# Optimization experiments

Measured on AMD Instinct MI355X. Metric: run time of the kernel, lower is better.

Reference implementation:

```python
import jax, jax.numpy as jnp
import numpy as np

N_HEADS = 16
N_KV_HEADS = 4
HEAD_DIM = 128


def setup_inputs() -> dict:
    key = jax.random.key(0)
    ks = jax.random.split(key, 5)
    B, T, C = 4, 2048, 2048
    kv_dim = N_KV_HEADS * HEAD_DIM
    s = 0.02
    return {
        "x": jax.random.normal(ks[0], (B, T, C), jnp.float32),
        "Wq": jax.random.normal(ks[1], (C, C), jnp.float32) * s,
        "Wk": jax.random.normal(ks[2], (kv_dim, C), jnp.float32) * s,
        "Wv": jax.random.normal(ks[3], (kv_dim, C), jnp.float32) * s,
        "Wo": jax.random.normal(ks[4], (C, C), jnp.float32) * s,
    }


def reference(x, Wq, Wk, Wv, Wo):
    B, T, C = x.shape
    n_rep = N_HEADS // N_KV_HEADS
    # projections (nn.Linear: y = x @ W^T), reshape to (B, H, T, D)
    q = (x @ Wq.T).reshape(B, T, N_HEADS, HEAD_DIM).transpose(0, 2, 1, 3)
    k = (x @ Wk.T).reshape(B, T, N_KV_HEADS, HEAD_DIM).transpose(0, 2, 1, 3)
    v = (x @ Wv.T).reshape(B, T, N_KV_HEADS, HEAD_DIM).transpose(0, 2, 1, 3)
    # GQA: expand kv heads (repeat_interleave on head dim)
    k = jnp.repeat(k, n_rep, axis=1)
    v = jnp.repeat(v, n_rep, axis=1)
    scale = 1.0 / np.sqrt(HEAD_DIM).astype(np.float32)
    scores = jnp.einsum("bhqd,bhkd->bhqk", q, k) * scale
    causal = jnp.tril(jnp.ones((T, T), bool))
    scores = jnp.where(causal[None, None], scores, -jnp.inf)
    attn = jax.nn.softmax(scores, axis=-1)  # dropout p=0 -> identity
    out = jnp.einsum("bhqk,bhkd->bhqd", attn, v)
    out = out.transpose(0, 2, 1, 3).reshape(B, T, C)
    return out @ Wo.T
```

## Files before the change

### kernel.cpp

```cpp
#include <hip/hip_runtime.h>

#define TB 4
#define TT 2048
#define TC 2048
#define NH 16
#define NKV 4
#define HD 128
#define KVDIM (NKV*HD)
#define NQKV (TC + 2*KVDIM)
#define MTOK (TB*TT)

typedef __bf16 bf16x8 __attribute__((ext_vector_type(8)));
typedef __bf16 bf16x2 __attribute__((ext_vector_type(2)));
typedef float  f32x4  __attribute__((ext_vector_type(4)));
typedef float  f32x16 __attribute__((ext_vector_type(16)));
typedef unsigned short ushort_t;
typedef unsigned short us8 __attribute__((ext_vector_type(8)));
typedef unsigned short us4 __attribute__((ext_vector_type(4)));
typedef unsigned int u32x4 __attribute__((ext_vector_type(4)));
typedef unsigned int u32x2 __attribute__((ext_vector_type(2)));

#define QSC 0.12751743f

__device__ __forceinline__ ushort_t f2bf(float f) {
    unsigned u = __builtin_bit_cast(unsigned, f);
    u += 0x7fffu + ((u >> 16) & 1u);
    return (ushort_t)(u >> 16);
}

__device__ __forceinline__ unsigned pkbf(float lo, float hi) {
    bf16x2 v;
    v[0] = (__bf16)lo; v[1] = (__bf16)hi;
    return __builtin_bit_cast(unsigned, v);
}

__device__ __forceinline__ void gload16(const ushort_t* g, ushort_t* l) {
    __builtin_amdgcn_global_load_lds(
        (const __attribute__((address_space(1))) unsigned int*)g,
        (__attribute__((address_space(3))) unsigned int*)l, 16, 0, 0);
}

__global__ __launch_bounds__(256) void cast_all(const float* __restrict__ x,
                                                const float* __restrict__ Wq,
                                                const float* __restrict__ Wk,
                                                const float* __restrict__ Wv,
                                                const float* __restrict__ Wo,
                                                ushort_t* __restrict__ dst) {
    const long E0 = 16777216;
    const long E1 = 20971520;
    const long E2 = 22020096;
    const long E3 = 23068672;
    const long E4 = 27262976;
    long i = (long)blockIdx.x * blockDim.x + threadIdx.x;
    long stride = (long)gridDim.x * blockDim.x;
    for (long e = i * 4; e < E4; e += stride * 4) {
        const float* src; long off;
        if (e < E0)      { src = x;  off = e; }
        else if (e < E1) { src = Wq; off = e - E0; }
        else if (e < E2) { src = Wk; off = e - E1; }
        else if (e < E3) { src = Wv; off = e - E2; }
        else             { src = Wo; off = e - E3; }
        float4 v = *reinterpret_cast<const float4*>(src + off);
        us4 o;
        o[0] = f2bf(v.x); o[1] = f2bf(v.y); o[2] = f2bf(v.z); o[3] = f2bf(v.w);
        *reinterpret_cast<us4*>(dst + e) = o;
    }
}

#define LBLK 8192

template<bool OUTF32, bool QSCALE>
__global__ __launch_bounds__(512, 2) void gemm256(const ushort_t* __restrict__ A,
                                                  const ushort_t* __restrict__ Bw,
                                                  float* __restrict__ Cf,
                                                  ushort_t* __restrict__ Cb,
                                                  int M, int N, int Kd, int nbn) {
    extern __shared__ ushort_t lds[];
    const int tid = threadIdx.x;
    const int lane = tid & 63, wid = tid >> 6;
    const int wm = wid >> 2, wn = wid & 3;
    const int g = lane >> 4, l16 = lane & 15;

    const int cpx = gridDim.x >> 3;
    const int swz = (blockIdx.x & 7) * cpx + (blockIdx.x >> 3);
    const int bm = swz / nbn, bn = swz % nbn;

    const ushort_t* Ag = A  + (size_t)bm * 256 * Kd;
    const ushort_t* Bg = Bw + (size_t)bn * 256 * Kd;

    const int r0 = tid >> 3;
    const int p0 = (tid & 7) ^ (r0 & 7);
    const size_t so0 = (size_t)r0 * Kd + p0 * 8;
    const size_t so1 = so0 + (size_t)64 * Kd;
    const int ldsw0 = wid * 512;

    f32x4 acc[8][4] = {};
    bf16x8 aA[4][2], bB[2][2];

    const int NK = Kd >> 6;
    const int NI = Kd >> 7;

#define STAGE(mat, half, tile) do { if ((tile) < NK) {                                   \
    const ushort_t* sg_ = ((mat) ? Bg : Ag) + (size_t)(half) * 128 * Kd + (size_t)(tile) * 64; \
    ushort_t* lb_ = lds + (((((tile)&1)*2 + (mat))*2 + (half)) * LBLK) + ldsw0;          \
    gload16(sg_ + so0, lb_);                                                             \
    gload16(sg_ + so1, lb_ + 4096);                                                      \
} } while(0)

#define LDA(buf, qm) do {                                                                \
    const ushort_t* Ah_ = lds + (((buf)*2 + 0)*2 + wm) * LBLK;                           \
    _Pragma("unroll") for (int mi_ = 0; mi_ < 4; mi_++) {                                \
        const int r_ = (qm)*64 + mi_*16 + l16;                                           \
        _Pragma("unroll") for (int ks_ = 0; ks_ < 2; ks_++)                              \
            aA[mi_][ks_] = *reinterpret_cast<const bf16x8*>(                             \
                Ah_ + r_*64 + (((ks_*4 + g) ^ (r_ & 7)) * 8));                           \
    }                                                                                    \
} while(0)

#define LDB(buf, qn) do {                                                                \
    const ushort_t* Bh_ = lds + (((buf)*2 + 1)*2 + (wn >> 1)) * LBLK;                    \
    _Pragma("unroll") for (int nj_ = 0; nj_ < 2; nj_++) {                                \
        const int r_ = (wn & 1)*64 + (qn)*32 + nj_*16 + l16;                             \
        _Pragma("unroll") for (int ks_ = 0; ks_ < 2; ks_++)                              \
            bB[nj_][ks_] = *reinterpret_cast<const bf16x8*>(                             \
                Bh_ + r_*64 + (((ks_*4 + g) ^ (r_ & 7)) * 8));                           \
    }                                                                                    \
} while(0)

#define MM(qm, qn) do {                                                                  \
    __builtin_amdgcn_s_setprio(1);                                                       \
    _Pragma("unroll") for (int mi_ = 0; mi_ < 4; mi_++)                                  \
    _Pragma("unroll") for (int nj_ = 0; nj_ < 2; nj_++)                                  \
    _Pragma("unroll") for (int ks_ = 0; ks_ < 2; ks_++)                                  \
        acc[(qm)*4 + mi_][(qn)*2 + nj_] = __builtin_amdgcn_mfma_f32_16x16x32_bf16(       \
            aA[mi_][ks_], bB[nj_][ks_], acc[(qm)*4 + mi_][(qn)*2 + nj_], 0, 0, 0);       \
    __builtin_amdgcn_s_setprio(0);                                                       \
} while(0)

#define PH_MID() do {                                                                    \
    __builtin_amdgcn_s_barrier();                                                        \
    asm volatile("s_waitcnt lgkmcnt(0)" ::: "memory");                                   \
    __builtin_amdgcn_sched_barrier(0);                                                   \
} while(0)

#define PH_END() __builtin_amdgcn_s_barrier()
#define PH_END_VM4() do { asm volatile("s_waitcnt vmcnt(4)" ::: "memory");               \
                          __builtin_amdgcn_s_barrier(); } while(0)
#define PH_END_VM0() do { asm volatile("s_waitcnt vmcnt(0)" ::: "memory");               \
                          __builtin_amdgcn_s_barrier(); } while(0)

    STAGE(0, 0, 0); STAGE(0, 1, 0); STAGE(1, 0, 0); STAGE(1, 1, 0);
    STAGE(0, 0, 1); STAGE(0, 1, 1);
    asm volatile("s_waitcnt vmcnt(4)" ::: "memory");
    __builtin_amdgcn_s_barrier();

    for (int i = 0; i < NI; ++i) {
        const int t0 = 2 * i, t1 = 2 * i + 1;
        const bool last = (i == NI - 1);
        LDA(0, 0); LDB(0, 0);
        STAGE(1, 0, t1); STAGE(1, 1, t1);
        PH_MID(); MM(0, 0); PH_END();
        LDB(0, 1);
        PH_MID(); MM(0, 1); PH_END();
        LDA(0, 1); LDB(0, 0);
        PH_MID(); MM(1, 0); PH_END();
        LDB(0, 1);
        STAGE(0, 0, t0 + 2); STAGE(0, 1, t0 + 2);
        PH_MID(); MM(1, 1);
        if (last) PH_END_VM0(); else PH_END_VM4();
        LDA(1, 0); LDB(1, 0);
        STAGE(1, 0, t0 + 2); STAGE(1, 1, t0 + 2);
        PH_MID(); MM(0, 0); PH_END();
        LDB(1, 1);
        PH_MID(); MM(0, 1); PH_END();
        LDA(1, 1); LDB(1, 0);
        PH_MID(); MM(1, 0); PH_END();
        LDB(1, 1);
        STAGE(0, 0, t1 + 2); STAGE(0, 1, t1 + 2);
        PH_MID(); MM(1, 1);
        if (last) PH_END_VM0(); else PH_END_VM4();
    }

#pragma unroll
    for (int mi = 0; mi < 8; mi++)
#pragma unroll
        for (int nj = 0; nj < 4; nj++) {
            const int rbase = bm * 256 + wm * 128 + mi * 16 + g * 4;
            const int col   = bn * 256 + wn * 64 + nj * 16 + l16;
#pragma unroll
            for (int r = 0; r < 4; r++) {
                float v = acc[mi][nj][r];
                if (QSCALE && col < TC) v *= QSC;
                size_t off = (size_t)(rbase + r) * N + col;
                if (OUTF32) Cf[off] = v;
                else        Cb[off] = __builtin_bit_cast(ushort_t, (__bf16)v);
            }
        }
#undef STAGE
#undef LDA
#undef LDB
#undef MM
#undef PH_MID
#undef PH_END
#undef PH_END_VM4
#undef PH_END_VM0
}

template<bool OUTF32, bool QSCALE>
__global__ __launch_bounds__(512, 2) void gemm_bk32(const ushort_t* __restrict__ A,
                                                    const ushort_t* __restrict__ Bw,
                                                    float* __restrict__ Cf,
                                                    ushort_t* __restrict__ Cb,
                                                    int N, int Kd, int nbn) {
    extern __shared__ ushort_t lds[];
    const int tid = threadIdx.x;
    const int lane = tid & 63, wid = tid >> 6;
    const int wm = wid >> 2, wn = wid & 3;
    const int g = lane >> 4, l16 = lane & 15;

    const int cpx = gridDim.x >> 3;
    const int swz = (blockIdx.x & 7) * cpx + (blockIdx.x >> 3);
    const int bm = swz / nbn, bn = swz % nbn;

    const ushort_t* Ag = A  + (size_t)bm * 128 * Kd;
    const ushort_t* Bg = Bw + (size_t)bn * 256 * Kd;

    const int arow = tid >> 2;
    const int apos = (tid & 3) ^ (arow & 3);
    const size_t aso  = (size_t)arow * Kd + apos * 8;
    const size_t bso0 = aso;
    const size_t bso1 = aso + (size_t)128 * Kd;
    const int ldsw = wid * 512;

    f32x4 acc[4][4] = {};
    bf16x8 aA[4], bB[4];
    const int NK = Kd >> 5;

#define STG(tile, bb) do { if ((tile) < NK) {                                            \
    const ushort_t* a_ = Ag + (size_t)(tile) * 32;                                       \
    const ushort_t* b_ = Bg + (size_t)(tile) * 32;                                       \
    ushort_t* lb_ = lds + (bb) * 12288 + ldsw;                                           \
    gload16(a_ + aso,  lb_);                                                             \
    gload16(b_ + bso0, lb_ + 4096);                                                      \
    gload16(b_ + bso1, lb_ + 8192);                                                      \
} } while(0)

#define LDAB(bb) do {                                                                    \
    const ushort_t* Ah_ = lds + (bb) * 12288;                                            \
    const ushort_t* Bh_ = Ah_ + 4096;                                                    \
    _Pragma("unroll") for (int mi_ = 0; mi_ < 4; mi_++) {                                \
        const int r_ = wm * 64 + mi_ * 16 + l16;                                         \
        aA[mi_] = *reinterpret_cast<const bf16x8*>(Ah_ + r_ * 32 + ((g ^ (r_ & 3)) * 8));\
    }                                                                                    \
    _Pragma("unroll") for (int nj_ = 0; nj_ < 4; nj_++) {                                \
        const int r_ = wn * 64 + nj_ * 16 + l16;                                         \
        bB[nj_] = *reinterpret_cast<const bf16x8*>(Bh_ + r_ * 32 + ((g ^ (r_ & 3)) * 8));\
    }                                                                                    \
} while(0)

    STG(0, 0); STG(1, 1);
    asm volatile("s_waitcnt vmcnt(3)" ::: "memory");
    __builtin_amdgcn_s_barrier();

    int cb = 0;
    for (int t = 0; t < NK; ++t) {
        const int sb = (cb == 0) ? 2 : cb - 1;
        STG(t + 2, sb);
        LDAB(cb);
        asm volatile("s_waitcnt lgkmcnt(0)" ::: "memory");
        __builtin_amdgcn_sched_barrier(0);
        __builtin_amdgcn_s_setprio(1);
#pragma unroll
        for (int mi = 0; mi < 4; mi++)
#pragma unroll
            for (int nj = 0; nj < 4; nj++)
                acc[mi][nj] = __builtin_amdgcn_mfma_f32_16x16x32_bf16(
                    aA[mi], bB[nj], acc[mi][nj], 0, 0, 0);
        __builtin_amdgcn_s_setprio(0);
        if (t + 2 < NK) asm volatile("s_waitcnt vmcnt(3)" ::: "memory");
        else            asm volatile("s_waitcnt vmcnt(0)" ::: "memory");
        __builtin_amdgcn_s_barrier();
        cb = (cb == 2) ? 0 : cb + 1;
    }

#pragma unroll
    for (int mi = 0; mi < 4; mi++)
#pragma unroll
        for (int nj = 0; nj < 4; nj++) {
            const int rbase = bm * 128 + wm * 64 + mi * 16 + g * 4;
            const int col   = bn * 256 + wn * 64 + nj * 16 + l16;
#pragma unroll
            for (int r = 0; r < 4; r++) {
                float v = acc[mi][nj][r];
                if (QSCALE && col < TC) v *= QSC;
                size_t off = (size_t)(rbase + r) * N + col;
                if (OUTF32) Cf[off] = v;
                else        Cb[off] = __builtin_bit_cast(ushort_t, (__bf16)v);
            }
        }
#undef STG
#undef LDAB
}

#define AQB 128
#define AKB 64
#define NTB (TT/AQB)
#define VTS 72

__global__ __launch_bounds__(256, 2) void attn_kernel(const ushort_t* __restrict__ qkv,
                                                      ushort_t* __restrict__ aout) {
    __shared__ alignas(16) ushort_t Ks[AKB * HD];
    __shared__ alignas(16) ushort_t Vt[HD * VTS];

    const int tid  = threadIdx.x;
    const int lane = tid & 63, wid = tid >> 6;
    const int hi   = lane >> 5, l31 = lane & 31;
    const int gx   = blockIdx.x;
    const int h    = blockIdx.y;
    const int b    = blockIdx.z;
    const int hk   = h >> 2;
    const size_t rowbase = (size_t)b * TT;

    const ushort_t* kg = qkv + TC + hk * HD;
    const ushort_t* vg = qkv + TC + KVDIM + hk * HD;
    const int rswz = (l31 & 7) << 3;

    us8 sk0, sk1, sk2, sk3;
    unsigned vv2[16];
    const int kr = tid >> 2, dcK = (tid & 3) * 32;
    const int vs = ((lane >> 2) & 7) << 3;

    for (int phase = 0; phase < 2; ++phase) {
        const int qb = (phase == 0 ? (NTB - 1 - gx) : gx) * AQB;
        const int q0 = qb + wid * 32;
        const int qrow = q0 + l31;

        bf16x8 qfr[8];
        {
            const ushort_t* qp = qkv + (rowbase + qrow) * NQKV + h * HD + hi * 8;
#pragma unroll
            for (int s = 0; s < 8; s++)
                qfr[s] = *reinterpret_cast<const bf16x8*>(qp + s * 16);
        }

        f32x16 oacc[4];
#pragma unroll
        for (int d = 0; d < 4; d++)
#pragma unroll
            for (int r = 0; r < 16; r++) oacc[d][r] = 0.f;
        float lsum = 0.f;

        const int ntiles = qb / AKB + 2;

        {
            const ushort_t* ksrc = kg + (rowbase + kr) * NQKV + dcK;
            sk0 = *reinterpret_cast<const us8*>(ksrc);
            sk1 = *reinterpret_cast<const us8*>(ksrc + 8);
            sk2 = *reinterpret_cast<const us8*>(ksrc + 16);
            sk3 = *reinterpret_cast<const us8*>(ksrc + 24);
            const ushort_t* vsrc = vg + (rowbase + wid * 16) * NQKV + 2 * lane;
#pragma unroll
            for (int j = 0; j < 16; j++)
                vv2[j] = *reinterpret_cast<const unsigned*>(vsrc + (size_t)j * NQKV);
        }

        for (int t = 0; t < ntiles; ++t) {
            const int kp0 = t * AKB;
            {
                const int kb = kr * HD + dcK, ksw = (kr & 7) << 3;
                *reinterpret_cast<us8*>(&Ks[(kb     ) ^ ksw]) = sk0;
                *reinterpret_cast<us8*>(&Ks[(kb +  8) ^ ksw]) = sk1;
                *reinterpret_cast<us8*>(&Ks[(kb + 16) ^ ksw]) = sk2;
                *reinterpret_cast<us8*>(&Ks[(kb + 24) ^ ksw]) = sk3;
                u32x4 pl0, ph0, pl1, ph1;
#pragma unroll
                for (int k = 0; k < 4; k++) {
                    pl0[k] = __builtin_amdgcn_perm(vv2[2 * k + 1], vv2[2 * k], 0x05040100u);
                    ph0[k] = __builtin_amdgcn_perm(vv2[2 * k + 1], vv2[2 * k], 0x07060302u);
                    pl1[k] = __builtin_amdgcn_perm(vv2[8 + 2 * k + 1], vv2[8 + 2 * k], 0x05040100u);
                    ph1[k] = __builtin_amdgcn_perm(vv2[8 + 2 * k + 1], vv2[8 + 2 * k], 0x07060302u);
                }
                ushort_t* r0p = &Vt[(2 * lane) * VTS];
                ushort_t* r1p = &Vt[(2 * lane + 1) * VTS];
                const int o0 = (wid * 16) ^ vs, o1 = (wid * 16 + 8) ^ vs;
                *reinterpret_cast<u32x4*>(r0p + o0) = pl0;
                *reinterpret_cast<u32x4*>(r0p + o1) = pl1;
                *reinterpret_cast<u32x4*>(r1p + o0) = ph0;
                *reinterpret_cast<u32x4*>(r1p + o1) = ph1;
            }
            if (t + 1 < ntiles) {
                const int kn = (t + 1) * AKB;
                const ushort_t* ksrc = kg + (rowbase + kn + kr) * NQKV + dcK;
                sk0 = *reinterpret_cast<const us8*>(ksrc);
                sk1 = *reinterpret_cast<const us8*>(ksrc + 8);
                sk2 = *reinterpret_cast<const us8*>(ksrc + 16);
                sk3 = *reinterpret_cast<const us8*>(ksrc + 24);
                const ushort_t* vsrc = vg + (rowbase + kn + wid * 16) * NQKV + 2 * lane;
#pragma unroll
                for (int j = 0; j < 16; j++)
                    vv2[j] = *reinterpret_cast<const unsigned*>(vsrc + (size_t)j * NQKV);
            }
            __syncthreads();

            if (kp0 <= q0 + 31) {
                f32x16 s0, s1;
#pragma unroll
                for (int r = 0; r < 16; r++) { s0[r] = 0.f; s1[r] = 0.f; }
                __builtin_amdgcn_s_setprio(1);
#pragma unroll
                for (int ds = 0; ds < 8; ds++) {
                    bf16x8 ka = *reinterpret_cast<const bf16x8*>(
                        &Ks[(l31 * HD + ds * 16 + hi * 8) ^ rswz]);
                    s0 = __builtin_amdgcn_mfma_f32_32x32x16_bf16(ka, qfr[ds], s0, 0, 0, 0);
                }
#pragma unroll
                for (int ds = 0; ds < 8; ds++) {
                    bf16x8 ka = *reinterpret_cast<const bf16x8*>(
                        &Ks[((32 + l31) * HD + ds * 16 + hi * 8) ^ rswz]);
                    s1 = __builtin_amdgcn_mfma_f32_32x32x16_bf16(ka, qfr[ds], s1, 0, 0, 0);
                }
                __builtin_amdgcn_s_setprio(0);
                if (kp0 + 63 > q0) {
#pragma unroll
                    for (int r = 0; r < 16; r++) {
                        int k0i = kp0 + (r & 3) + 8 * (r >> 2) + 4 * hi;
                        if (k0i > qrow)      s0[r] = -1e30f;
                        if (k0i + 32 > qrow) s1[r] = -1e30f;
                    }
                }
                unsigned pk0[8], pk1[8];
                float ps = 0.f;
#pragma unroll
                for (int w = 0; w < 8; w++) {
                    float a0 = exp2f(s0[2 * w]), a1 = exp2f(s0[2 * w + 1]);
                    float b0 = exp2f(s1[2 * w]), b1 = exp2f(s1[2 * w + 1]);
                    ps += (a0 + a1) + (b0 + b1);
                    pk0[w] = pkbf(a0, a1);
                    pk1[w] = pkbf(b0, b1);
                }
                ps += __shfl_xor(ps, 32);
                lsum += ps;
                __builtin_amdgcn_s_setprio(1);
#pragma unroll
                for (int ks = 0; ks < 4; ks++) {
                    const unsigned* pkt = (ks < 2) ? pk0 : pk1;
                    unsigned c00 = pkt[4 * (ks & 1) + 0];
                    unsigned c01 = pkt[4 * (ks & 1) + 1];
                    unsigned c10 = pkt[4 * (ks & 1) + 2];
                    unsigned c11 = pkt[4 * (ks & 1) + 3];
                    u32x2 rA = __builtin_amdgcn_permlane32_swap(c00, c10, false, false);
                    u32x2 rB = __builtin_amdgcn_permlane32_swap(c01, c11, false, false);
                    u32x4 faw;
                    faw[0] = rA[0];
                    faw[1] = rB[0];
                    faw[2] = rA[1];
                    faw[3] = rB[1];
                    bf16x8 pa = __builtin_bit_cast(bf16x8, faw);
#pragma unroll
                    for (int dt = 0; dt < 4; dt++) {
                        int doff = dt * 32 + l31;
                        int sr = ((doff >> 3) & 7) << 3;
                        bf16x8 vb = *reinterpret_cast<const bf16x8*>(
                            &Vt[doff * VTS + ((ks * 16 + hi * 8) ^ sr)]);
                        oacc[dt] = __builtin_amdgcn_mfma_f32_32x32x16_bf16(vb, pa, oacc[dt], 0, 0, 0);
                    }
                }
                __builtin_amdgcn_s_setprio(0);
            }
            __syncthreads();
        }

        const float rl = 1.f / lsum;
        ushort_t* orow = aout + (rowbase + qrow) * TC + h * HD;
#pragma unroll
        for (int dt = 0; dt < 4; dt++)
#pragma unroll
            for (int rp = 0; rp < 8; rp++) {
                int d = dt * 32 + ((2 * rp) & 3) + 8 * ((2 * rp) >> 2) + 4 * hi;
                unsigned w = pkbf(oacc[dt][2 * rp] * rl, oacc[dt][2 * rp + 1] * rl);
                *reinterpret_cast<unsigned*>(orow + d) = w;
            }
    }
}

extern "C" void kernel_launch(void* const* d_in, const int* in_sizes, int n_in,
                              void* d_out, int out_size, void* d_ws, size_t ws_size,
                              hipStream_t stream) {
    const float* x  = (const float*)d_in[0];
    const float* Wq = (const float*)d_in[1];
    const float* Wk = (const float*)d_in[2];
    const float* Wv = (const float*)d_in[3];
    const float* Wo = (const float*)d_in[4];
    float* out = (float*)d_out;

    ushort_t* x_bf  = (ushort_t*)d_ws;
    ushort_t* wqkv  = x_bf  + (size_t)MTOK * TC;
    ushort_t* wo_bf = wqkv  + (size_t)NQKV * TC;
    ushort_t* qkv   = wo_bf + (size_t)TC * TC;
    ushort_t* attn  = x_bf;

    cast_all<<<4096, 256, 0, stream>>>(x, Wq, Wk, Wv, Wo, x_bf);

    const int GK_LDS  = 73728;
    const int G256_LDS = 131072;
    hipFuncSetAttribute(reinterpret_cast<const void*>(gemm_bk32<false, true>),
                        hipFuncAttributeMaxDynamicSharedMemorySize, GK_LDS);
    hipFuncSetAttribute(reinterpret_cast<const void*>(gemm256<true, false>),
                        hipFuncAttributeMaxDynamicSharedMemorySize, G256_LDS);

    gemm_bk32<false, true><<<dim3(768), 512, GK_LDS, stream>>>(
        x_bf, wqkv, nullptr, qkv, NQKV, TC, 12);

    attn_kernel<<<dim3(NTB / 2, NH, TB), 256, 0, stream>>>(qkv, attn);

    gemm256<true, false><<<dim3(256), 512, G256_LDS, stream>>>(
        attn, wo_bf, out, nullptr, MTOK, TC, TC, TC / 256);
}
```

Baseline: 319.5 us.

## Double-buffer attention K/V tiles with direct global-to-LDS K loads

```diff
diff --git a/kernel.cpp b/kernel.cpp
--- a/kernel.cpp
+++ b/kernel.cpp
@@ -309,8 +309,8 @@
 
 __global__ __launch_bounds__(256, 2) void attn_kernel(const ushort_t* __restrict__ qkv,
                                                       ushort_t* __restrict__ aout) {
-    __shared__ alignas(16) ushort_t Ks[AKB * HD];
-    __shared__ alignas(16) ushort_t Vt[HD * VTS];
+    __shared__ alignas(16) ushort_t Ks[2][AKB * HD];
+    __shared__ alignas(16) ushort_t Vt[2][HD * VTS];
 
     const int tid  = threadIdx.x;
     const int lane = tid & 63, wid = tid >> 6;
@@ -325,10 +325,22 @@
     const ushort_t* vg = qkv + TC + KVDIM + hk * HD;
     const int rswz = (l31 & 7) << 3;
 
-    us8 sk0, sk1, sk2, sk3;
+    const int rr = tid >> 4;
+    const int ksrcc = ((tid & 15) ^ (rr & 7)) * 8;
     unsigned vv2[16];
-    const int kr = tid >> 2, dcK = (tid & 3) * 32;
     const int vs = ((lane >> 2) & 7) << 3;
+
+#define ISSK(kp, cur_) do {                                                              \
+    _Pragma("unroll") for (int c_ = 0; c_ < 4; c_++)                                     \
+        gload16(kg + (size_t)(rowbase + (kp) + c_ * 16 + rr) * NQKV + ksrcc,             \
+                &Ks[cur_][c_ * 2048 + wid * 512]);                                       \
+} while(0)
+
+#define ISSV(kp) do {                                                                    \
+    const ushort_t* vsrc_ = vg + (rowbase + (kp) + wid * 16) * NQKV + 2 * lane;          \
+    _Pragma("unroll") for (int j_ = 0; j_ < 16; j_++)                                    \
+        vv2[j_] = *reinterpret_cast<const unsigned*>(vsrc_ + (size_t)j_ * NQKV);         \
+} while(0)
 
     for (int phase = 0; phase < 2; ++phase) {
         const int qb = (phase == 0 ? (NTB - 1 - gx) : gx) * AQB;
@@ -352,26 +364,14 @@
 
         const int ntiles = qb / AKB + 2;
 
-        {
-            const ushort_t* ksrc = kg + (rowbase + kr) * NQKV + dcK;
-            sk0 = *reinterpret_cast<const us8*>(ksrc);
-            sk1 = *reinterpret_cast<const us8*>(ksrc + 8);
-            sk2 = *reinterpret_cast<const us8*>(ksrc + 16);
-            sk3 = *reinterpret_cast<const us8*>(ksrc + 24);
-            const ushort_t* vsrc = vg + (rowbase + wid * 16) * NQKV + 2 * lane;
-#pragma unroll
-            for (int j = 0; j < 16; j++)
-                vv2[j] = *reinterpret_cast<const unsigned*>(vsrc + (size_t)j * NQKV);
-        }
+        if (phase) __syncthreads();
+        ISSV(0);
+        ISSK(0, 0);
 
         for (int t = 0; t < ntiles; ++t) {
             const int kp0 = t * AKB;
+            const int cur = t & 1;
             {
-                const int kb = kr * HD + dcK, ksw = (kr & 7) << 3;
-                *reinterpret_cast<us8*>(&Ks[(kb     ) ^ ksw]) = sk0;
-                *reinterpret_cast<us8*>(&Ks[(kb +  8) ^ ksw]) = sk1;
-                *reinterpret_cast<us8*>(&Ks[(kb + 16) ^ ksw]) = sk2;
-                *reinterpret_cast<us8*>(&Ks[(kb + 24) ^ ksw]) = sk3;
                 u32x4 pl0, ph0, pl1, ph1;
 #pragma unroll
                 for (int k = 0; k < 4; k++) {
@@ -380,27 +380,20 @@
                     pl1[k] = __builtin_amdgcn_perm(vv2[8 + 2 * k + 1], vv2[8 + 2 * k], 0x05040100u);
                     ph1[k] = __builtin_amdgcn_perm(vv2[8 + 2 * k + 1], vv2[8 + 2 * k], 0x07060302u);
                 }
-                ushort_t* r0p = &Vt[(2 * lane) * VTS];
-                ushort_t* r1p = &Vt[(2 * lane + 1) * VTS];
+                ushort_t* r0p = &Vt[cur][(2 * lane) * VTS];
+                ushort_t* r1p = &Vt[cur][(2 * lane + 1) * VTS];
                 const int o0 = (wid * 16) ^ vs, o1 = (wid * 16 + 8) ^ vs;
                 *reinterpret_cast<u32x4*>(r0p + o0) = pl0;
                 *reinterpret_cast<u32x4*>(r0p + o1) = pl1;
                 *reinterpret_cast<u32x4*>(r1p + o0) = ph0;
                 *reinterpret_cast<u32x4*>(r1p + o1) = ph1;
             }
+            __syncthreads();
+
             if (t + 1 < ntiles) {
-                const int kn = (t + 1) * AKB;
-                const ushort_t* ksrc = kg + (rowbase + kn + kr) * NQKV + dcK;
-                sk0 = *reinterpret_cast<const us8*>(ksrc);
-                sk1 = *reinterpret_cast<const us8*>(ksrc + 8);
-                sk2 = *reinterpret_cast<const us8*>(ksrc + 16);
-                sk3 = *reinterpret_cast<const us8*>(ksrc + 24);
-                const ushort_t* vsrc = vg + (rowbase + kn + wid * 16) * NQKV + 2 * lane;
-#pragma unroll
-                for (int j = 0; j < 16; j++)
-                    vv2[j] = *reinterpret_cast<const unsigned*>(vsrc + (size_t)j * NQKV);
+                ISSV((t + 1) * AKB);
+                ISSK((t + 1) * AKB, cur ^ 1);
             }
-            __syncthreads();
 
             if (kp0 <= q0 + 31) {
                 f32x16 s0, s1;
@@ -410,13 +403,13 @@
 #pragma unroll
                 for (int ds = 0; ds < 8; ds++) {
                     bf16x8 ka = *reinterpret_cast<const bf16x8*>(
-                        &Ks[(l31 * HD + ds * 16 + hi * 8) ^ rswz]);
+                        &Ks[cur][(l31 * HD + ds * 16 + hi * 8) ^ rswz]);
                     s0 = __builtin_amdgcn_mfma_f32_32x32x16_bf16(ka, qfr[ds], s0, 0, 0, 0);
                 }
 #pragma unroll
                 for (int ds = 0; ds < 8; ds++) {
                     bf16x8 ka = *reinterpret_cast<const bf16x8*>(
-                        &Ks[((32 + l31) * HD + ds * 16 + hi * 8) ^ rswz]);
+                        &Ks[cur][((32 + l31) * HD + ds * 16 + hi * 8) ^ rswz]);
                     s1 = __builtin_amdgcn_mfma_f32_32x32x16_bf16(ka, qfr[ds], s1, 0, 0, 0);
                 }
                 __builtin_amdgcn_s_setprio(0);
@@ -461,13 +454,12 @@
                         int doff = dt * 32 + l31;
                         int sr = ((doff >> 3) & 7) << 3;
                         bf16x8 vb = *reinterpret_cast<const bf16x8*>(
-                            &Vt[doff * VTS + ((ks * 16 + hi * 8) ^ sr)]);
+                            &Vt[cur][doff * VTS + ((ks * 16 + hi * 8) ^ sr)]);
                         oacc[dt] = __builtin_amdgcn_mfma_f32_32x32x16_bf16(vb, pa, oacc[dt], 0, 0, 0);
                     }
                 }
                 __builtin_amdgcn_s_setprio(0);
             }
-            __syncthreads();
         }
 
         const float rl = 1.f / lsum;
@@ -481,6 +473,8 @@
                 *reinterpret_cast<unsigned*>(orow + d) = w;
             }
     }
+#undef ISSK
+#undef ISSV
 }
 
 extern "C" void kernel_launch(void* const* d_in, const int* in_sizes, int n_in,
```

New measurement: 315.8 us. About the same (-1.2%).

## Split QKV projection into 256-tile Q GEMM and bk32 KV GEMM; double-buffer attention LDS

Applied to the files above, without the earlier changes.

```diff
diff --git a/kernel.cpp b/kernel.cpp
--- a/kernel.cpp
+++ b/kernel.cpp
@@ -74,7 +74,7 @@
                                                   const ushort_t* __restrict__ Bw,
                                                   float* __restrict__ Cf,
                                                   ushort_t* __restrict__ Cb,
-                                                  int M, int N, int Kd, int nbn) {
+                                                  int Nld, int Kd, int nbn) {
     extern __shared__ ushort_t lds[];
     const int tid = threadIdx.x;
     const int lane = tid & 63, wid = tid >> 6;
@@ -190,8 +190,8 @@
 #pragma unroll
             for (int r = 0; r < 4; r++) {
                 float v = acc[mi][nj][r];
-                if (QSCALE && col < TC) v *= QSC;
-                size_t off = (size_t)(rbase + r) * N + col;
+                if (QSCALE) v *= QSC;
+                size_t off = (size_t)(rbase + r) * Nld + col;
                 if (OUTF32) Cf[off] = v;
                 else        Cb[off] = __builtin_bit_cast(ushort_t, (__bf16)v);
             }
@@ -206,12 +206,10 @@
 #undef PH_END_VM0
 }
 
-template<bool OUTF32, bool QSCALE>
 __global__ __launch_bounds__(512, 2) void gemm_bk32(const ushort_t* __restrict__ A,
                                                     const ushort_t* __restrict__ Bw,
-                                                    float* __restrict__ Cf,
                                                     ushort_t* __restrict__ Cb,
-                                                    int N, int Kd, int nbn) {
+                                                    int Nld, int Kd, int nbn) {
     extern __shared__ ushort_t lds[];
     const int tid = threadIdx.x;
     const int lane = tid & 63, wid = tid >> 6;
@@ -290,13 +288,9 @@
             const int rbase = bm * 128 + wm * 64 + mi * 16 + g * 4;
             const int col   = bn * 256 + wn * 64 + nj * 16 + l16;
 #pragma unroll
-            for (int r = 0; r < 4; r++) {
-                float v = acc[mi][nj][r];
-                if (QSCALE && col < TC) v *= QSC;
-                size_t off = (size_t)(rbase + r) * N + col;
-                if (OUTF32) Cf[off] = v;
-                else        Cb[off] = __builtin_bit_cast(ushort_t, (__bf16)v);
-            }
+            for (int r = 0; r < 4; r++)
+                Cb[(size_t)(rbase + r) * Nld + col] =
+                    __builtin_bit_cast(ushort_t, (__bf16)acc[mi][nj][r]);
         }
 #undef STG
 #undef LDAB
@@ -309,8 +303,8 @@
 
 __global__ __launch_bounds__(256, 2) void attn_kernel(const ushort_t* __restrict__ qkv,
                                                       ushort_t* __restrict__ aout) {
-    __shared__ alignas(16) ushort_t Ks[AKB * HD];
-    __shared__ alignas(16) ushort_t Vt[HD * VTS];
+    __shared__ alignas(16) ushort_t Ks[2][AKB * HD];
+    __shared__ alignas(16) ushort_t Vt[2][HD * VTS];
 
     const int tid  = threadIdx.x;
     const int lane = tid & 63, wid = tid >> 6;
@@ -363,15 +357,17 @@
             for (int j = 0; j < 16; j++)
                 vv2[j] = *reinterpret_cast<const unsigned*>(vsrc + (size_t)j * NQKV);
         }
+        if (phase) __syncthreads();
 
         for (int t = 0; t < ntiles; ++t) {
             const int kp0 = t * AKB;
+            const int cur = t & 1;
             {
                 const int kb = kr * HD + dcK, ksw = (kr & 7) << 3;
-                *reinterpret_cast<us8*>(&Ks[(kb     ) ^ ksw]) = sk0;
-                *reinterpret_cast<us8*>(&Ks[(kb +  8) ^ ksw]) = sk1;
-                *reinterpret_cast<us8*>(&Ks[(kb + 16) ^ ksw]) = sk2;
-                *reinterpret_cast<us8*>(&Ks[(kb + 24) ^ ksw]) = sk3;
+                *reinterpret_cast<us8*>(&Ks[cur][(kb     ) ^ ksw]) = sk0;
+                *reinterpret_cast<us8*>(&Ks[cur][(kb +  8) ^ ksw]) = sk1;
+                *reinterpret_cast<us8*>(&Ks[cur][(kb + 16) ^ ksw]) = sk2;
+                *reinterpret_cast<us8*>(&Ks[cur][(kb + 24) ^ ksw]) = sk3;
                 u32x4 pl0, ph0, pl1, ph1;
 #pragma unroll
                 for (int k = 0; k < 4; k++) {
@@ -380,8 +376,8 @@
                     pl1[k] = __builtin_amdgcn_perm(vv2[8 + 2 * k + 1], vv2[8 + 2 * k], 0x05040100u);
                     ph1[k] = __builtin_amdgcn_perm(vv2[8 + 2 * k + 1], vv2[8 + 2 * k], 0x07060302u);
                 }
-                ushort_t* r0p = &Vt[(2 * lane) * VTS];
-                ushort_t* r1p = &Vt[(2 * lane + 1) * VTS];
+                ushort_t* r0p = &Vt[cur][(2 * lane) * VTS];
+                ushort_t* r1p = &Vt[cur][(2 * lane + 1) * VTS];
                 const int o0 = (wid * 16) ^ vs, o1 = (wid * 16 + 8) ^ vs;
                 *reinterpret_cast<u32x4*>(r0p + o0) = pl0;
                 *reinterpret_cast<u32x4*>(r0p + o1) = pl1;
@@ -410,13 +406,13 @@
 #pragma unroll
                 for (int ds = 0; ds < 8; ds++) {
                     bf16x8 ka = *reinterpret_cast<const bf16x8*>(
-                        &Ks[(l31 * HD + ds * 16 + hi * 8) ^ rswz]);
+                        &Ks[cur][(l31 * HD + ds * 16 + hi * 8) ^ rswz]);
                     s0 = __builtin_amdgcn_mfma_f32_32x32x16_bf16(ka, qfr[ds], s0, 0, 0, 0);
                 }
 #pragma unroll
                 for (int ds = 0; ds < 8; ds++) {
                     bf16x8 ka = *reinterpret_cast<const bf16x8*>(
-                        &Ks[((32 + l31) * HD + ds * 16 + hi * 8) ^ rswz]);
+                        &Ks[cur][((32 + l31) * HD + ds * 16 + hi * 8) ^ rswz]);
                     s1 = __builtin_amdgcn_mfma_f32_32x32x16_bf16(ka, qfr[ds], s1, 0, 0, 0);
                 }
                 __builtin_amdgcn_s_setprio(0);
@@ -461,13 +457,12 @@
                         int doff = dt * 32 + l31;
                         int sr = ((doff >> 3) & 7) << 3;
                         bf16x8 vb = *reinterpret_cast<const bf16x8*>(
-                            &Vt[doff * VTS + ((ks * 16 + hi * 8) ^ sr)]);
+                            &Vt[cur][doff * VTS + ((ks * 16 + hi * 8) ^ sr)]);
                         oacc[dt] = __builtin_amdgcn_mfma_f32_32x32x16_bf16(vb, pa, oacc[dt], 0, 0, 0);
                     }
                 }
                 __builtin_amdgcn_s_setprio(0);
             }
-            __syncthreads();
         }
 
         const float rl = 1.f / lsum;
@@ -501,18 +496,23 @@
 
     cast_all<<<4096, 256, 0, stream>>>(x, Wq, Wk, Wv, Wo, x_bf);
 
-    const int GK_LDS  = 73728;
+    const int GK_LDS   = 73728;
     const int G256_LDS = 131072;
-    hipFuncSetAttribute(reinterpret_cast<const void*>(gemm_bk32<false, true>),
+    hipFuncSetAttribute(reinterpret_cast<const void*>(gemm_bk32),
                         hipFuncAttributeMaxDynamicSharedMemorySize, GK_LDS);
+    hipFuncSetAttribute(reinterpret_cast<const void*>(gemm256<false, true>),
+                        hipFuncAttributeMaxDynamicSharedMemorySize, G256_LDS);
     hipFuncSetAttribute(reinterpret_cast<const void*>(gemm256<true, false>),
                         hipFuncAttributeMaxDynamicSharedMemorySize, G256_LDS);
 
-    gemm_bk32<false, true><<<dim3(768), 512, GK_LDS, stream>>>(
-        x_bf, wqkv, nullptr, qkv, NQKV, TC, 12);
+    gemm256<false, true><<<dim3(256), 512, G256_LDS, stream>>>(
+        x_bf, wqkv, nullptr, qkv, NQKV, TC, 8);
+
+    gemm_bk32<<<dim3(256), 512, GK_LDS, stream>>>(
+        x_bf, wqkv + (size_t)TC * TC, qkv + TC, NQKV, TC, 4);
 
     attn_kernel<<<dim3(NTB / 2, NH, TB), 256, 0, stream>>>(qkv, attn);
 
     gemm256<true, false><<<dim3(256), 512, G256_LDS, stream>>>(
-        attn, wo_bf, out, nullptr, MTOK, TC, TC, TC / 256);
-}
+        attn, wo_bf, out, nullptr, TC, TC, 8);
+}
```

Result: no change. 319.6 us (+0.0%).
